# Performance work log

Measured on AMD Instinct MI355X. Metric: run time of the kernel, lower is better.

## Reference

```python
import jax, jax.numpy as jnp
import numpy as np

N_TOKENS = 8192
D_MODEL = 1024
D_FF = 4096
N_EXPERTS = 8


def setup_inputs() -> dict:
    key = jax.random.key(0)
    ks = jax.random.split(key, 5)
    scale_in = 1.0 / np.sqrt(D_MODEL)
    x = jax.random.normal(ks[0], (N_TOKENS, D_MODEL), dtype=jnp.float32)
    gate_w = jax.random.normal(ks[1], (D_MODEL, N_EXPERTS), dtype=jnp.float32) * scale_in
    gate_b = jnp.zeros((N_EXPERTS,), dtype=jnp.float32)
    expert_w = jax.random.normal(ks[2], (N_EXPERTS, D_MODEL, D_FF), dtype=jnp.float32) * scale_in
    expert_b = jnp.zeros((N_EXPERTS, D_FF), dtype=jnp.float32)
    return {"x": x, "gate_w": gate_w, "gate_b": gate_b, "expert_w": expert_w, "expert_b": expert_b}


def reference(x, gate_w, gate_b, expert_w, expert_b):
    # Gate: [N, E] logits -> softmax -> top-1 expert per token
    gate_logits = x @ gate_w + gate_b
    gate_probs = jax.nn.softmax(gate_logits, axis=-1)
    top1 = jnp.argmax(gate_probs, axis=-1)  # [N], == argsort(...)[:, -1]

    # Dense all-expert compute, as in the original: [E, N, d_ff]
    expert_outputs = jnp.einsum('nd,edf->enf', x, expert_w) + expert_b[:, None, :]

    # Gather each token's top-1 expert output: [N, d_ff]
    selected = expert_outputs[top1, jnp.arange(x.shape[0])]
    return selected
```

## Files before the change

### kernel.cpp

```cpp
#include <hip/hip_runtime.h>


#define N_TOKENS 8192
#define D_MODEL  1024
#define D_FF     4096
#define N_EXPERTS 8

#define BM 128
#define BN 128
#define BK 64
#define NKT (D_MODEL / BK)
#define MT_MAX (N_TOKENS / BM + N_EXPERTS)
#define NTILES (D_FF / BN)
#define GATE_BLOCKS (N_TOKENS / 4)
#define WCONV_BLOCKS ((D_FF / 64) * (D_MODEL / 256) * N_EXPERTS)

typedef float  floatx4 __attribute__((ext_vector_type(4)));
typedef short  short8  __attribute__((ext_vector_type(8)));

__device__ __forceinline__ unsigned short f2bf(float f) {
    union { float f; unsigned u; } a; a.f = f;
    return (unsigned short)((a.u + 0x7fffu + ((a.u >> 16) & 1u)) >> 16);
}

#define GLDS(gp, lp) __builtin_amdgcn_global_load_lds( \
    (const __attribute__((address_space(1))) unsigned int*)(const void*)(gp), \
    (__attribute__((address_space(3))) unsigned int*)(void*)(lp), 16, 0, 0)

__global__ __launch_bounds__(256) void gate_kernel(
    const float* __restrict__ x, const float* __restrict__ gw,
    const float* __restrict__ gb,
    unsigned short* __restrict__ xb, int* __restrict__ top1)
{
    int wave = threadIdx.x >> 6;
    int l    = threadIdx.x & 63;
    int n = blockIdx.x * 4 + wave;
    const float4* xr = (const float4*)(x + (size_t)n * D_MODEL);
    float acc[N_EXPERTS];
#pragma unroll
    for (int e = 0; e < N_EXPERTS; ++e) acc[e] = 0.f;
#pragma unroll
    for (int j = 0; j < 4; ++j) {
        int d4 = j * 64 + l;
        float4 v = xr[d4];
        float vv[4] = { v.x, v.y, v.z, v.w };
#pragma unroll
        for (int t = 0; t < 4; ++t) {
            const float4* g = (const float4*)(gw + (size_t)(d4 * 4 + t) * N_EXPERTS);
            float4 g0 = g[0], g1 = g[1];
            acc[0] += vv[t] * g0.x; acc[1] += vv[t] * g0.y;
            acc[2] += vv[t] * g0.z; acc[3] += vv[t] * g0.w;
            acc[4] += vv[t] * g1.x; acc[5] += vv[t] * g1.y;
            acc[6] += vv[t] * g1.z; acc[7] += vv[t] * g1.w;
        }
        union { unsigned short us[4]; uint2 u; } pk;
        pk.us[0] = f2bf(v.x); pk.us[1] = f2bf(v.y);
        pk.us[2] = f2bf(v.z); pk.us[3] = f2bf(v.w);
        ((uint2*)(xb + (size_t)n * D_MODEL))[d4] = pk.u;
    }
#pragma unroll
    for (int e = 0; e < N_EXPERTS; ++e)
        for (int off = 32; off > 0; off >>= 1)
            acc[e] += __shfl_down(acc[e], off);
    if (l == 0) {
        float best = acc[0] + gb[0]; int be = 0;
#pragma unroll
        for (int e = 1; e < N_EXPERTS; ++e) {
            float v = acc[e] + gb[e];
            if (v > best) { best = v; be = e; }
        }
        top1[n] = be;
    }
}

#define WST2 260
__global__ __launch_bounds__(256) void wconv_kernel(
    const float* __restrict__ ew, unsigned short* __restrict__ wt)
{
    __shared__ unsigned short tt[64 * WST2];
    int b  = blockIdx.x;
    int f0 = (b & 63) * 64;
    int d0 = ((b >> 6) & 3) * 256;
    int e  = b >> 8;
    int t  = threadIdx.x;
    const float* we = ew + (size_t)e * D_MODEL * D_FF + (size_t)d0 * D_FF + f0;
    int fg = (t & 15) * 4;
    int dg = (t >> 4) * 16;
    unsigned short v[4][16];
#pragma unroll
    for (int j = 0; j < 16; ++j) {
        float4 r = *(const float4*)(we + (size_t)(dg + j) * D_FF + fg);
        v[0][j] = f2bf(r.x); v[1][j] = f2bf(r.y);
        v[2][j] = f2bf(r.z); v[3][j] = f2bf(r.w);
    }
#pragma unroll
    for (int i = 0; i < 4; ++i) {
#pragma unroll
        for (int p = 0; p < 4; ++p) {
            union { unsigned short us[4]; uint2 u; } pk;
            pk.us[0] = v[i][p*4+0]; pk.us[1] = v[i][p*4+1];
            pk.us[2] = v[i][p*4+2]; pk.us[3] = v[i][p*4+3];
            *(uint2*)&tt[(size_t)(fg + i) * WST2 + dg + p * 4] = pk.u;
        }
    }
    __syncthreads();
    unsigned short* wte = wt + (size_t)e * D_FF * D_MODEL + (size_t)f0 * D_MODEL + d0;
    int fr = t >> 5;
    int cr = (t & 31) * 8;
#pragma unroll
    for (int p = 0; p < 8; ++p) {
        int f = fr + p * 8;
        uint2 a = *(const uint2*)&tt[(size_t)f * WST2 + cr];
        uint2 c = *(const uint2*)&tt[(size_t)f * WST2 + cr + 4];
        uint4 o; o.x = a.x; o.y = a.y; o.z = c.x; o.w = c.y;
        *(uint4*)(wte + (size_t)f * D_MODEL + cr) = o;
    }
}

__global__ __launch_bounds__(1024) void route_kernel(
    const int* __restrict__ top1, int* __restrict__ tile_expert, int* __restrict__ list)
{
    __shared__ int wtot[16][N_EXPERTS];
    __shared__ int wbase[16][N_EXPERTS];
    __shared__ int pofs[N_EXPERTS];
    int t = threadIdx.x, wv = t >> 6, l = t & 63;

    for (int i = t; i < MT_MAX * BM; i += 1024) list[i] = -1;

    int e8[8];
    const int4* tp = (const int4*)(top1 + t * 8);
    int4 a = tp[0], b = tp[1];
    e8[0] = a.x; e8[1] = a.y; e8[2] = a.z; e8[3] = a.w;
    e8[4] = b.x; e8[5] = b.y; e8[6] = b.z; e8[7] = b.w;
    int c[N_EXPERTS], s[N_EXPERTS];
#pragma unroll
    for (int e = 0; e < N_EXPERTS; ++e) c[e] = 0;
#pragma unroll
    for (int j = 0; j < 8; ++j) c[e8[j]]++;
#pragma unroll
    for (int e = 0; e < N_EXPERTS; ++e) s[e] = c[e];
    for (int off = 1; off < 64; off <<= 1) {
#pragma unroll
        for (int e = 0; e < N_EXPERTS; ++e) {
            int v = __shfl_up(s[e], off);
            if (l >= off) s[e] += v;
        }
    }
    if (l == 63)
#pragma unroll
        for (int e = 0; e < N_EXPERTS; ++e) wtot[wv][e] = s[e];
    __syncthreads();
    if (t == 0) {
        int cnt[N_EXPERTS];
        for (int e = 0; e < N_EXPERTS; ++e) {
            cnt[e] = 0;
            for (int w = 0; w < 16; ++w) { wbase[w][e] = cnt[e]; cnt[e] += wtot[w][e]; }
        }
        int off = 0;
        for (int e = 0; e < N_EXPERTS; ++e) {
            pofs[e] = off;
            int ntl = (cnt[e] + BM - 1) / BM;
            for (int k = 0; k < ntl; ++k) tile_expert[off / BM + k] = e;
            off += ntl * BM;
        }
        for (int k = off / BM; k < MT_MAX; ++k) tile_expert[k] = -1;
    }
    __syncthreads();
    int base[N_EXPERTS];
#pragma unroll
    for (int e = 0; e < N_EXPERTS; ++e) base[e] = pofs[e] + wbase[wv][e] + s[e] - c[e];
#pragma unroll
    for (int j = 0; j < 8; ++j) {
        int e = e8[j];
        list[base[e]++] = t * 8 + j;
    }
}

__global__ __launch_bounds__(256) void gemm_kernel(
    const unsigned short* __restrict__ xb,
    const unsigned short* __restrict__ wt,
    const float* __restrict__ eb,
    const int* __restrict__ tile_expert,
    const int* __restrict__ list,
    float* __restrict__ out)
{
    int bid = blockIdx.x;
    int xcd = bid & 7, w = bid >> 3;
    int mt  = w >> 2;
    int nt  = (xcd << 2) | (w & 3);
    int e = tile_expert[mt];
    if (e < 0) return;
    int n0 = nt * BN;

    __shared__ unsigned short As[2][BM * BK];
    __shared__ unsigned short Bs[2][BN * BK];
    __shared__ int toks[BM];

    int tid = threadIdx.x;
    int lane = tid & 63, wave = tid >> 6;
    if (tid < BM) toks[tid] = list[mt * BM + tid];
    __syncthreads();

    const unsigned short* gA[4];
    const unsigned short* gB[4];
    const unsigned short* wbase = wt + (size_t)e * D_FF * D_MODEL;
#pragma unroll
    for (int i = 0; i < 4; ++i) {
        int s = wave * 256 + i * 64 + lane;
        int row = s >> 3, c8 = (s & 7) ^ (row & 7);
        int ta = toks[row]; if (ta < 0) ta = 0;
        gA[i] = xb + (size_t)ta * D_MODEL + c8 * 8;
        gB[i] = wbase + (size_t)(n0 + row) * D_MODEL + c8 * 8;
    }

    auto stage = [&](int b, int kt) {
        int k0 = kt * BK;
        unsigned short* ap = &As[b][0];
        unsigned short* bp = &Bs[b][0];
#pragma unroll
        for (int i = 0; i < 4; ++i) GLDS(gA[i] + k0, ap + (size_t)(wave * 256 + i * 64) * 8);
#pragma unroll
        for (int i = 0; i < 4; ++i) GLDS(gB[i] + k0, bp + (size_t)(wave * 256 + i * 64) * 8);
    };

    floatx4 acc[4][4];
#pragma unroll
    for (int mi = 0; mi < 4; ++mi)
#pragma unroll
        for (int ni = 0; ni < 4; ++ni)
            acc[mi][ni] = (floatx4){0.f, 0.f, 0.f, 0.f};

    int mw = (wave >> 1) * 64;
    int nw = (wave & 1) * 64;
    int q = lane >> 4, r = lane & 15;
    int xr = r & 7;
    int ra[4], rb[4];
#pragma unroll
    for (int i = 0; i < 4; ++i) { ra[i] = (mw + i * 16 + r) * 8; rb[i] = (nw + i * 16 + r) * 8; }

    stage(0, 0);
    stage(1, 1);
    asm volatile("s_waitcnt vmcnt(8)" ::: "memory");
    __builtin_amdgcn_s_barrier();
    __builtin_amdgcn_sched_barrier(0);

    for (int kt = 0; kt < NKT; ++kt) {
        int cur = kt & 1;
        const unsigned short* Ac = &As[cur][0];
        const unsigned short* Bc = &Bs[cur][0];
#pragma unroll
        for (int ks = 0; ks < 2; ++ks) {
            int cq = (ks * 4 + q) ^ xr;
            short8 af[4], bf[4];
#pragma unroll
            for (int mi = 0; mi < 4; ++mi)
                af[mi] = *(const short8*)&Ac[(size_t)(ra[mi] + cq) * 8];
#pragma unroll
            for (int ni = 0; ni < 4; ++ni)
                bf[ni] = *(const short8*)&Bc[(size_t)(rb[ni] + cq) * 8];
#pragma unroll
            for (int mi = 0; mi < 4; ++mi)
#pragma unroll
                for (int ni = 0; ni < 4; ++ni)
                    acc[mi][ni] = __builtin_amdgcn_mfma_f32_16x16x32_bf16(
                        af[mi], bf[ni], acc[mi][ni], 0, 0, 0);
        }
        __builtin_amdgcn_sched_barrier(0);
        __builtin_amdgcn_s_barrier();
        if (kt + 2 < NKT) {
            stage(cur, kt + 2);
            asm volatile("s_waitcnt vmcnt(8)" ::: "memory");
        } else {
            asm volatile("s_waitcnt vmcnt(0)" ::: "memory");
        }
        __builtin_amdgcn_s_barrier();
        __builtin_amdgcn_sched_barrier(0);
    }

#pragma unroll
    for (int ni = 0; ni < 4; ++ni) {
        int f = n0 + nw + ni * 16 + r;
        float bias = eb[(size_t)e * D_FF + f];
#pragma unroll
        for (int mi = 0; mi < 4; ++mi) {
            int mbase = mw + mi * 16 + q * 4;
#pragma unroll
            for (int i = 0; i < 4; ++i) {
                int tok = toks[mbase + i];
                if (tok >= 0) out[(size_t)tok * D_FF + f] = acc[mi][ni][i] + bias;
            }
        }
    }
}

extern "C" void kernel_launch(void* const* d_in, const int* in_sizes, int n_in,
                              void* d_out, int out_size, void* d_ws, size_t ws_size,
                              hipStream_t stream) {
    const float* x  = (const float*)d_in[0];
    const float* gw = (const float*)d_in[1];
    const float* gb = (const float*)d_in[2];
    const float* ew = (const float*)d_in[3];
    const float* eb = (const float*)d_in[4];
    float* out = (float*)d_out;

    char* ws = (char*)d_ws;
    int* top1        = (int*)ws;
    int* tile_expert = (int*)(ws + 32768);
    int* list        = (int*)(ws + 36864);
    unsigned short* xb = (unsigned short*)(ws + 131072);
    unsigned short* wt = (unsigned short*)(ws + 131072 + (size_t)N_TOKENS * D_MODEL * 2);

    hipLaunchKernelGGL(gate_kernel, dim3(GATE_BLOCKS), dim3(256), 0, stream,
                       x, gw, gb, xb, top1);
    hipLaunchKernelGGL(wconv_kernel, dim3(WCONV_BLOCKS), dim3(256), 0, stream,
                       ew, wt);
    hipLaunchKernelGGL(route_kernel, dim3(1), dim3(1024), 0, stream,
                       top1, tile_expert, list);
    hipLaunchKernelGGL(gemm_kernel, dim3(MT_MAX * NTILES), dim3(256), 0, stream,
                       xb, wt, eb, tile_expert, list, out);
}
```

Baseline: 440.7 us.

## Switch gemm to BK=32 triple-buffered LDS pipeline for higher occupancy

Halves the K tile to 32 and moves from two to three LDS buffers, which shrinks shared memory per block so three blocks can fit per CU (launch bounds now request 3). The XOR swizzle is reworked for 4 chunks per row, and the wait counts are adjusted so two tiles stay in flight. The aim is better latency hiding through more resident blocks and a deeper prefetch. In exchange there are twice as many barrier iterations with half the MFMA work each, and the occupancy hint may limit registers for the 64 accumulators.

Result: faster. 423.0 us (-4.0%).

```diff
diff --git a/kernel.cpp b/kernel.cpp
--- a/kernel.cpp
+++ b/kernel.cpp
@@ -8,8 +8,9 @@
 
 #define BM 128
 #define BN 128
-#define BK 64
+#define BK 32
 #define NKT (D_MODEL / BK)
+#define NBUF 3
 #define MT_MAX (N_TOKENS / BM + N_EXPERTS)
 #define NTILES (D_FF / BN)
 #define GATE_BLOCKS (N_TOKENS / 4)
@@ -176,7 +177,7 @@
     }
 }
 
-__global__ __launch_bounds__(256) void gemm_kernel(
+__global__ __launch_bounds__(256, 3) void gemm_kernel(
     const unsigned short* __restrict__ xb,
     const unsigned short* __restrict__ wt,
     const float* __restrict__ eb,
@@ -192,8 +193,8 @@
     if (e < 0) return;
     int n0 = nt * BN;
 
-    __shared__ unsigned short As[2][BM * BK];
-    __shared__ unsigned short Bs[2][BN * BK];
+    __shared__ unsigned short As[NBUF][BM * BK];
+    __shared__ unsigned short Bs[NBUF][BN * BK];
     __shared__ int toks[BM];
 
     int tid = threadIdx.x;
@@ -201,13 +202,14 @@
     if (tid < BM) toks[tid] = list[mt * BM + tid];
     __syncthreads();
 
-    const unsigned short* gA[4];
-    const unsigned short* gB[4];
+    const unsigned short* gA[2];
+    const unsigned short* gB[2];
     const unsigned short* wbase = wt + (size_t)e * D_FF * D_MODEL;
 #pragma unroll
-    for (int i = 0; i < 4; ++i) {
-        int s = wave * 256 + i * 64 + lane;
-        int row = s >> 3, c8 = (s & 7) ^ (row & 7);
+    for (int i = 0; i < 2; ++i) {
+        int s = wave * 128 + i * 64 + lane;
+        int row = s >> 2;
+        int c8 = (s & 3) ^ (row & 3) ^ ((row >> 2) & 3);
         int ta = toks[row]; if (ta < 0) ta = 0;
         gA[i] = xb + (size_t)ta * D_MODEL + c8 * 8;
         gB[i] = wbase + (size_t)(n0 + row) * D_MODEL + c8 * 8;
@@ -218,9 +220,9 @@
         unsigned short* ap = &As[b][0];
         unsigned short* bp = &Bs[b][0];
 #pragma unroll
-        for (int i = 0; i < 4; ++i) GLDS(gA[i] + k0, ap + (size_t)(wave * 256 + i * 64) * 8);
-#pragma unroll
-        for (int i = 0; i < 4; ++i) GLDS(gB[i] + k0, bp + (size_t)(wave * 256 + i * 64) * 8);
+        for (int i = 0; i < 2; ++i) GLDS(gA[i] + k0, ap + (size_t)(wave * 128 + i * 64) * 8);
+#pragma unroll
+        for (int i = 0; i < 2; ++i) GLDS(gB[i] + k0, bp + (size_t)(wave * 128 + i * 64) * 8);
     };
 
     floatx4 acc[4][4];
@@ -233,48 +235,52 @@
     int mw = (wave >> 1) * 64;
     int nw = (wave & 1) * 64;
     int q = lane >> 4, r = lane & 15;
-    int xr = r & 7;
-    int ra[4], rb[4];
-#pragma unroll
-    for (int i = 0; i < 4; ++i) { ra[i] = (mw + i * 16 + r) * 8; rb[i] = (nw + i * 16 + r) * 8; }
+    int pa[4], pb[4];
+#pragma unroll
+    for (int i = 0; i < 4; ++i) {
+        int rowA = mw + i * 16 + r;
+        pa[i] = rowA * BK + ((q ^ (rowA & 3) ^ ((rowA >> 2) & 3)) * 8);
+        int rowB = nw + i * 16 + r;
+        pb[i] = rowB * BK + ((q ^ (rowB & 3) ^ ((rowB >> 2) & 3)) * 8);
+    }
 
     stage(0, 0);
     stage(1, 1);
+    stage(2, 2);
     asm volatile("s_waitcnt vmcnt(8)" ::: "memory");
     __builtin_amdgcn_s_barrier();
     __builtin_amdgcn_sched_barrier(0);
 
+    int cur = 0;
     for (int kt = 0; kt < NKT; ++kt) {
-        int cur = kt & 1;
         const unsigned short* Ac = &As[cur][0];
         const unsigned short* Bc = &Bs[cur][0];
-#pragma unroll
-        for (int ks = 0; ks < 2; ++ks) {
-            int cq = (ks * 4 + q) ^ xr;
-            short8 af[4], bf[4];
-#pragma unroll
-            for (int mi = 0; mi < 4; ++mi)
-                af[mi] = *(const short8*)&Ac[(size_t)(ra[mi] + cq) * 8];
+        short8 af[4], bf[4];
+#pragma unroll
+        for (int mi = 0; mi < 4; ++mi)
+            af[mi] = *(const short8*)&Ac[pa[mi]];
+#pragma unroll
+        for (int ni = 0; ni < 4; ++ni)
+            bf[ni] = *(const short8*)&Bc[pb[ni]];
+#pragma unroll
+        for (int mi = 0; mi < 4; ++mi)
 #pragma unroll
             for (int ni = 0; ni < 4; ++ni)
-                bf[ni] = *(const short8*)&Bc[(size_t)(rb[ni] + cq) * 8];
-#pragma unroll
-            for (int mi = 0; mi < 4; ++mi)
-#pragma unroll
-                for (int ni = 0; ni < 4; ++ni)
-                    acc[mi][ni] = __builtin_amdgcn_mfma_f32_16x16x32_bf16(
-                        af[mi], bf[ni], acc[mi][ni], 0, 0, 0);
-        }
+                acc[mi][ni] = __builtin_amdgcn_mfma_f32_16x16x32_bf16(
+                    af[mi], bf[ni], acc[mi][ni], 0, 0, 0);
         __builtin_amdgcn_sched_barrier(0);
         __builtin_amdgcn_s_barrier();
-        if (kt + 2 < NKT) {
-            stage(cur, kt + 2);
+        if (kt + 3 < NKT) {
+            stage(cur, kt + 3);
             asm volatile("s_waitcnt vmcnt(8)" ::: "memory");
-        } else {
+        } else if (kt == NKT - 3) {
+            asm volatile("s_waitcnt vmcnt(4)" ::: "memory");
+        } else if (kt == NKT - 2) {
             asm volatile("s_waitcnt vmcnt(0)" ::: "memory");
         }
         __builtin_amdgcn_s_barrier();
         __builtin_amdgcn_sched_barrier(0);
+        cur = (cur == NBUF - 1) ? 0 : cur + 1;
     }
 
 #pragma unroll
```

## Enlarge expert GEMM tiles to 256x256 with 8-wave quadrant-pipelined schedule

Applied to the files above, without the earlier changes.

The grouped expert GEMM now uses 256x256 output tiles computed by 512 threads. Each wave owns a 128x64 sub-tile and works through it in four MFMA quadrants. Global-to-LDS loads of the next K-slice are split into halves and interleaved between the quadrants, with s_setprio raised around the MFMA bursts. The aim is more data reuse per loaded byte and better overlap of memory traffic with matrix math. The cost is more LDS (about 128KB per block), more barriers, fewer blocks in flight, and more padding waste per expert tile.

Result: slower. 642.1 us (+45.7%).

```diff
diff --git a/kernel.cpp b/kernel.cpp
--- a/kernel.cpp
+++ b/kernel.cpp
@@ -6,8 +6,8 @@
 #define D_FF     4096
 #define N_EXPERTS 8
 
-#define BM 128
-#define BN 128
+#define BM 256
+#define BN 256
 #define BK 64
 #define NKT (D_MODEL / BK)
 #define MT_MAX (N_TOKENS / BM + N_EXPERTS)
@@ -26,6 +26,8 @@
 #define GLDS(gp, lp) __builtin_amdgcn_global_load_lds( \
     (const __attribute__((address_space(1))) unsigned int*)(const void*)(gp), \
     (__attribute__((address_space(3))) unsigned int*)(void*)(lp), 16, 0, 0)
+
+#define MFMA16(a, b, c) __builtin_amdgcn_mfma_f32_16x16x32_bf16(a, b, c, 0, 0, 0)
 
 __global__ __launch_bounds__(256) void gate_kernel(
     const float* __restrict__ x, const float* __restrict__ gw,
@@ -176,7 +178,19 @@
     }
 }
 
-__global__ __launch_bounds__(256) void gemm_kernel(
+#define QUAD(AF, BF, MO, NO)                                                   \
+    __builtin_amdgcn_s_setprio(1);                                             \
+    _Pragma("unroll")                                                          \
+    for (int mi = 0; mi < 4; ++mi) {                                           \
+        _Pragma("unroll")                                                      \
+        for (int ni = 0; ni < 2; ++ni) {                                       \
+            acc[(MO)+mi][(NO)+ni] = MFMA16(AF[mi][0], BF[ni][0], acc[(MO)+mi][(NO)+ni]); \
+            acc[(MO)+mi][(NO)+ni] = MFMA16(AF[mi][1], BF[ni][1], acc[(MO)+mi][(NO)+ni]); \
+        }                                                                      \
+    }                                                                          \
+    __builtin_amdgcn_s_setprio(0);
+
+__global__ __launch_bounds__(512, 2) void gemm_kernel(
     const unsigned short* __restrict__ xb,
     const unsigned short* __restrict__ wt,
     const float* __restrict__ eb,
@@ -185,15 +199,15 @@
     float* __restrict__ out)
 {
     int bid = blockIdx.x;
-    int xcd = bid & 7, w = bid >> 3;
-    int mt  = w >> 2;
-    int nt  = (xcd << 2) | (w & 3);
+    int xcd = bid & 7, j = bid >> 3;
+    int mt  = j >> 1;
+    int nt  = (xcd << 1) | (j & 1);
     int e = tile_expert[mt];
     if (e < 0) return;
     int n0 = nt * BN;
 
-    __shared__ unsigned short As[2][BM * BK];
-    __shared__ unsigned short Bs[2][BN * BK];
+    __shared__ unsigned short As[2][2][128 * BK];
+    __shared__ unsigned short Bs[2][2][128 * BK];
     __shared__ int toks[BM];
 
     int tid = threadIdx.x;
@@ -201,89 +215,131 @@
     if (tid < BM) toks[tid] = list[mt * BM + tid];
     __syncthreads();
 
-    const unsigned short* gA[4];
-    const unsigned short* gB[4];
-    const unsigned short* wbase = wt + (size_t)e * D_FF * D_MODEL;
-#pragma unroll
-    for (int i = 0; i < 4; ++i) {
-        int s = wave * 256 + i * 64 + lane;
-        int row = s >> 3, c8 = (s & 7) ^ (row & 7);
-        int ta = toks[row]; if (ta < 0) ta = 0;
-        gA[i] = xb + (size_t)ta * D_MODEL + c8 * 8;
-        gB[i] = wbase + (size_t)(n0 + row) * D_MODEL + c8 * 8;
-    }
-
-    auto stage = [&](int b, int kt) {
-        int k0 = kt * BK;
-        unsigned short* ap = &As[b][0];
-        unsigned short* bp = &Bs[b][0];
-#pragma unroll
-        for (int i = 0; i < 4; ++i) GLDS(gA[i] + k0, ap + (size_t)(wave * 256 + i * 64) * 8);
-#pragma unroll
-        for (int i = 0; i < 4; ++i) GLDS(gB[i] + k0, bp + (size_t)(wave * 256 + i * 64) * 8);
+    int aoff[2][2], boff[2][2];
+    const unsigned short* wbp = wt + (size_t)e * D_FF * D_MODEL;
+#pragma unroll
+    for (int h = 0; h < 2; ++h)
+#pragma unroll
+        for (int i = 0; i < 2; ++i) {
+            int s = i * 512 + wave * 64 + lane;
+            int row = s >> 3, c8 = (s & 7) ^ (row & 7);
+            int ta = toks[h * 128 + row]; if (ta < 0) ta = 0;
+            aoff[h][i] = ta * D_MODEL + c8 * 8;
+            boff[h][i] = (n0 + h * 128 + row) * D_MODEL + c8 * 8;
+        }
+
+    auto stageA = [&](int b, int h, int kt) {
+        unsigned short* dst = &As[b][h][0];
+#pragma unroll
+        for (int i = 0; i < 2; ++i)
+            GLDS(xb + (size_t)aoff[h][i] + kt * BK, dst + (i * 512 + wave * 64) * 8);
     };
-
-    floatx4 acc[4][4];
-#pragma unroll
-    for (int mi = 0; mi < 4; ++mi)
+    auto stageB = [&](int b, int h, int kt) {
+        unsigned short* dst = &Bs[b][h][0];
+#pragma unroll
+        for (int i = 0; i < 2; ++i)
+            GLDS(wbp + (size_t)boff[h][i] + kt * BK, dst + (i * 512 + wave * 64) * 8);
+    };
+
+    floatx4 acc[8][4];
+#pragma unroll
+    for (int mi = 0; mi < 8; ++mi)
 #pragma unroll
         for (int ni = 0; ni < 4; ++ni)
             acc[mi][ni] = (floatx4){0.f, 0.f, 0.f, 0.f};
 
-    int mw = (wave >> 1) * 64;
-    int nw = (wave & 1) * 64;
+    int wr = wave >> 2, wc = wave & 3;
     int q = lane >> 4, r = lane & 15;
-    int xr = r & 7;
-    int ra[4], rb[4];
-#pragma unroll
-    for (int i = 0; i < 4; ++i) { ra[i] = (mw + i * 16 + r) * 8; rb[i] = (nw + i * 16 + r) * 8; }
-
-    stage(0, 0);
-    stage(1, 1);
-    asm volatile("s_waitcnt vmcnt(8)" ::: "memory");
+    int cq0 = ((0 * 4 + q) ^ (r & 7)) * 8;
+    int cq1 = ((1 * 4 + q) ^ (r & 7)) * 8;
+    int arow[8], brow[4];
+#pragma unroll
+    for (int i = 0; i < 8; ++i) arow[i] = (i * 16 + r) * BK;
+#pragma unroll
+    for (int i = 0; i < 4; ++i) brow[i] = ((wc & 1) * 64 + i * 16 + r) * BK;
+    const unsigned short* Abase[2] = { &As[0][wr][0], &As[1][wr][0] };
+    const unsigned short* Bbase[2] = { &Bs[0][wc >> 1][0], &Bs[1][wc >> 1][0] };
+
+    stageA(0, 0, 0); stageA(0, 1, 0); stageB(0, 0, 0); stageB(0, 1, 0);
+    stageA(1, 0, 1); stageA(1, 1, 1);
+    asm volatile("s_waitcnt vmcnt(4)" ::: "memory");
     __builtin_amdgcn_s_barrier();
     __builtin_amdgcn_sched_barrier(0);
 
+    short8 af0[4][2], af1[4][2], bf0[2][2], bf1[2][2];
+
     for (int kt = 0; kt < NKT; ++kt) {
-        int cur = kt & 1;
-        const unsigned short* Ac = &As[cur][0];
-        const unsigned short* Bc = &Bs[cur][0];
-#pragma unroll
-        for (int ks = 0; ks < 2; ++ks) {
-            int cq = (ks * 4 + q) ^ xr;
-            short8 af[4], bf[4];
-#pragma unroll
-            for (int mi = 0; mi < 4; ++mi)
-                af[mi] = *(const short8*)&Ac[(size_t)(ra[mi] + cq) * 8];
-#pragma unroll
-            for (int ni = 0; ni < 4; ++ni)
-                bf[ni] = *(const short8*)&Bc[(size_t)(rb[ni] + cq) * 8];
-#pragma unroll
-            for (int mi = 0; mi < 4; ++mi)
-#pragma unroll
-                for (int ni = 0; ni < 4; ++ni)
-                    acc[mi][ni] = __builtin_amdgcn_mfma_f32_16x16x32_bf16(
-                        af[mi], bf[ni], acc[mi][ni], 0, 0, 0);
-        }
-        __builtin_amdgcn_sched_barrier(0);
-        __builtin_amdgcn_s_barrier();
+        int b = kt & 1;
+        const unsigned short* A = Abase[b];
+        const unsigned short* B = Bbase[b];
+
+#pragma unroll
+        for (int mi = 0; mi < 4; ++mi) {
+            af0[mi][0] = *(const short8*)&A[arow[mi] + cq0];
+            af0[mi][1] = *(const short8*)&A[arow[mi] + cq1];
+        }
+#pragma unroll
+        for (int ni = 0; ni < 2; ++ni) {
+            bf0[ni][0] = *(const short8*)&B[brow[ni] + cq0];
+            bf0[ni][1] = *(const short8*)&B[brow[ni] + cq1];
+        }
+        if (kt + 1 < NKT) stageB(b ^ 1, 0, kt + 1);
+        __builtin_amdgcn_sched_barrier(0);
+        __builtin_amdgcn_s_barrier();
+        asm volatile("s_waitcnt lgkmcnt(0)" ::: "memory");
+        __builtin_amdgcn_sched_barrier(0);
+        QUAD(af0, bf0, 0, 0)
+        __builtin_amdgcn_sched_barrier(0);
+        __builtin_amdgcn_s_barrier();
+
+#pragma unroll
+        for (int mi = 0; mi < 4; ++mi) {
+            af1[mi][0] = *(const short8*)&A[arow[4 + mi] + cq0];
+            af1[mi][1] = *(const short8*)&A[arow[4 + mi] + cq1];
+        }
+        if (kt + 1 < NKT) stageB(b ^ 1, 1, kt + 1);
+        __builtin_amdgcn_sched_barrier(0);
+        __builtin_amdgcn_s_barrier();
+        asm volatile("s_waitcnt lgkmcnt(0)" ::: "memory");
+        __builtin_amdgcn_sched_barrier(0);
+        QUAD(af1, bf0, 4, 0)
+        __builtin_amdgcn_sched_barrier(0);
+        __builtin_amdgcn_s_barrier();
+
+#pragma unroll
+        for (int ni = 0; ni < 2; ++ni) {
+            bf1[ni][0] = *(const short8*)&B[brow[2 + ni] + cq0];
+            bf1[ni][1] = *(const short8*)&B[brow[2 + ni] + cq1];
+        }
+        if (kt + 2 < NKT) stageA(b, 0, kt + 2);
+        __builtin_amdgcn_sched_barrier(0);
+        __builtin_amdgcn_s_barrier();
+        asm volatile("s_waitcnt lgkmcnt(0)" ::: "memory");
+        __builtin_amdgcn_sched_barrier(0);
+        QUAD(af1, bf1, 4, 2)
+        __builtin_amdgcn_sched_barrier(0);
+        __builtin_amdgcn_s_barrier();
+
         if (kt + 2 < NKT) {
-            stage(cur, kt + 2);
-            asm volatile("s_waitcnt vmcnt(8)" ::: "memory");
+            stageA(b, 1, kt + 2);
+            asm volatile("s_waitcnt vmcnt(4)" ::: "memory");
         } else {
             asm volatile("s_waitcnt vmcnt(0)" ::: "memory");
         }
-        __builtin_amdgcn_s_barrier();
-        __builtin_amdgcn_sched_barrier(0);
+        __builtin_amdgcn_sched_barrier(0);
+        __builtin_amdgcn_s_barrier();
+        QUAD(af0, bf1, 0, 2)
+        __builtin_amdgcn_sched_barrier(0);
+        __builtin_amdgcn_s_barrier();
     }
 
 #pragma unroll
     for (int ni = 0; ni < 4; ++ni) {
-        int f = n0 + nw + ni * 16 + r;
+        int f = n0 + wc * 64 + ni * 16 + r;
         float bias = eb[(size_t)e * D_FF + f];
 #pragma unroll
-        for (int mi = 0; mi < 4; ++mi) {
-            int mbase = mw + mi * 16 + q * 4;
+        for (int mi = 0; mi < 8; ++mi) {
+            int mbase = wr * 128 + mi * 16 + q * 4;
 #pragma unroll
             for (int i = 0; i < 4; ++i) {
                 int tok = toks[mbase + i];
@@ -316,6 +372,6 @@
                        ew, wt);
     hipLaunchKernelGGL(route_kernel, dim3(1), dim3(1024), 0, stream,
                        top1, tile_expert, list);
-    hipLaunchKernelGGL(gemm_kernel, dim3(MT_MAX * NTILES), dim3(256), 0, stream,
+    hipLaunchKernelGGL(gemm_kernel, dim3(MT_MAX * NTILES), dim3(512), 0, stream,
                        xb, wt, eb, tile_expert, list, out);
 }
```
